# Performance work log

Measured on AMD Instinct MI355X. Metric: run time of the kernel, lower is better.

Reference implementation:

```python
import jax, jax.numpy as jnp
import numpy as np

B, CIN, C, H, W = 2, 64, 128, 64, 1024
H2, W2 = H // 2, W // 2

def _unfold(x, k, pad, stride, dil=1):
    # F.unfold equivalent -> [B, C, k*k, Ho, Wo] with (kh, kw) row-major ordering
    Bx, Cx, Hx, Wx = x.shape
    Ho = (Hx + 2 * pad - dil * (k - 1) - 1) // stride + 1
    Wo = (Wx + 2 * pad - dil * (k - 1) - 1) // stride + 1
    xp = jnp.pad(x, ((0, 0), (0, 0), (pad, pad), (pad, pad)))
    pats = [xp[:, :, i * dil:i * dil + stride * (Ho - 1) + 1:stride,
                  j * dil:j * dil + stride * (Wo - 1) + 1:stride]
            for i in range(k) for j in range(k)]
    return jnp.stack(pats, axis=2)

def _conv(x, w, b, pad, dil=1):
    y = jax.lax.conv_general_dilated(x, w, (1, 1), ((pad, pad), (pad, pad)),
                                     rhs_dilation=(dil, dil),
                                     dimension_numbers=('NCHW', 'OIHW', 'NCHW'))
    return y + b[None, :, None, None]

def _c1x1(x, w, b):
    return jnp.einsum('oi,bi...->bo...', w, x) + b.reshape((1, -1) + (1,) * (x.ndim - 2))

def _bn(x, s, b):
    shp = (1, -1) + (1,) * (x.ndim - 2)
    return x * s.reshape(shp) + b.reshape(shp)

def _forward(x, xyz, c1_w, c1_b, c2_w, c2_b, c3_w, c3_b, c4_w, c4_b, c5_w, c5_b,
             rbn_s, rbn_b, p_w, p_b, pbn_s, pbn_b, lin_w, lin_b,
             w1_w, w1_b, w2_w, w2_b, w3_w, w3_b,
             wbn1_s, wbn1_b, wbn2_s, wbn2_b, wbn3_s, wbn3_b):
    lrelu, relu = jax.nn.leaky_relu, jax.nn.relu
    # get_group_mask geometry (kernel 5, stride 2): relative neighbor coordinates
    gxyz = _unfold(xyz, 5, 2, 2) - xyz[:, :, ::2, ::2][:, :, None]  # [B,3,25,H2,W2]
    # ResBlock trunk (eval-mode BN folded to per-channel scale/shift)
    shortcut = lrelu(_c1x1(x, c1_w, c1_b))
    resA1 = _bn(lrelu(_conv(x, c2_w, c2_b, pad=1)), rbn_s[0], rbn_b[0])
    resA2 = _bn(lrelu(_conv(resA1, c3_w, c3_b, pad=2, dil=2)), rbn_s[1], rbn_b[1])
    resA3 = _bn(lrelu(_conv(resA2, c4_w, c4_b, pad=1, dil=2)), rbn_s[2], rbn_b[2])
    concat = jnp.concatenate([resA1, resA2, resA3], axis=1)
    resA = _bn(lrelu(_c1x1(concat, c5_w, c5_b)), rbn_s[3], rbn_b[3]) + shortcut
    # PConv downsample: pointwise MLP, WeightNet on geometry, unfold + per-pixel matmul
    h = resA
    for i in range(3):
        h = relu(_bn(_c1x1(h, p_w[i], p_b[i]), pbn_s[i], pbn_b[i]))
    wn = relu(_bn(_c1x1(gxyz, w1_w, w1_b), wbn1_s, wbn1_b))
    wn = relu(_bn(_c1x1(wn, w2_w, w2_b), wbn2_s, wbn2_b))
    wn = relu(_bn(_c1x1(wn, w3_w, w3_b), wbn3_s, wbn3_b))          # [B,16,25,H2,W2]
    unf = _unfold(h, 5, 2, 2)                                      # [B,C,25,H2,W2]
    y = jnp.einsum('bckhw,bnkhw->bcnhw', unf, wn).reshape(B, C * 16, H2, W2)
    resB = relu(_bn(_c1x1(y, lin_w, lin_b), pbn_s[3], pbn_b[3]))   # [B,C,H2,W2]
    return resB, resA

def setup_inputs():
    keys = iter(jax.random.split(jax.random.key(0), 48))
    def rn(shape, scale=0.05):
        return jax.random.normal(next(keys), shape, jnp.float32) * scale
    def bn_pair(shape):
        return 1.0 + rn(shape, 0.1), rn(shape, 0.1)
    d = {}
    d['x'] = rn((B, CIN, H, W), 1.0)
    d['xyz'] = rn((B, 3, H, W), 0.1)
    d['c1_w'], d['c1_b'] = rn((C, CIN)), rn((C,))
    d['c2_w'], d['c2_b'] = rn((C, CIN, 3, 3)), rn((C,))
    d['c3_w'], d['c3_b'] = rn((C, C, 3, 3)), rn((C,))
    d['c4_w'], d['c4_b'] = rn((C, C, 2, 2)), rn((C,))
    d['c5_w'], d['c5_b'] = rn((C, 3 * C)), rn((C,))
    d['rbn_s'], d['rbn_b'] = bn_pair((4, C))
    d['p_w'], d['p_b'] = rn((3, C, C)), rn((3, C))
    d['pbn_s'], d['pbn_b'] = bn_pair((4, C))
    d['lin_w'], d['lin_b'] = rn((C, 16 * C), 0.02), rn((C,))
    d['w1_w'], d['w1_b'] = rn((8, 3), 0.5), rn((8,))
    d['w2_w'], d['w2_b'] = rn((8, 8), 0.5), rn((8,))
    d['w3_w'], d['w3_b'] = rn((16, 8), 0.5), rn((16,))
    d['wbn1_s'], d['wbn1_b'] = bn_pair((8,))
    d['wbn2_s'], d['wbn2_b'] = bn_pair((8,))
    d['wbn3_s'], d['wbn3_b'] = bn_pair((16,))
    return d

def reference(x, xyz, c1_w, c1_b, c2_w, c2_b, c3_w, c3_b, c4_w, c4_b, c5_w, c5_b,
              rbn_s, rbn_b, p_w, p_b, pbn_s, pbn_b, lin_w, lin_b,
              w1_w, w1_b, w2_w, w2_b, w3_w, w3_b,
              wbn1_s, wbn1_b, wbn2_s, wbn2_b, wbn3_s, wbn3_b):
    return _forward(x, xyz, c1_w, c1_b, c2_w, c2_b, c3_w, c3_b, c4_w, c4_b, c5_w, c5_b,
                    rbn_s, rbn_b, p_w, p_b, pbn_s, pbn_b, lin_w, lin_b,
                    w1_w, w1_b, w2_w, w2_b, w3_w, w3_b,
                    wbn1_s, wbn1_b, wbn2_s, wbn2_b, wbn3_s, wbn3_b)
```

## Files before the change

### kernel.cpp

```cpp
#include <hip/hip_runtime.h>
#include <hip/hip_bf16.h>

typedef __hip_bfloat16 bf16;
typedef unsigned short u16;
typedef unsigned int   u32;

#define B_   2
#define CIN_ 64
#define C_   128
#define H_   64
#define W_   1024
#define HW_  (H_*W_)
#define H2_  32
#define W2_  512
#define HW2_ (H2_*W2_)

typedef __attribute__((ext_vector_type(8))) short bf16x8;
typedef __attribute__((ext_vector_type(4))) float f32x4;

#define OFF_C2  0
#define OFF_C3  73728
#define OFF_C4  221184
#define OFF_C5  286720
#define OFF_C1  335872
#define OFF_PW  344064
#define OFF_LIN 393216
#define WTS_TOT 655360
__device__ __align__(16) u16 g_wts[WTS_TOT];
__device__ __align__(16) u16 g_b1[(size_t)B_*C_*HW_];
__device__ __align__(16) u16 g_b2[(size_t)B_*C_*HW_];
__device__ __align__(16) u16 g_b3[(size_t)B_*C_*HW_];
__device__ __align__(16) u16 g_xb[(size_t)B_*HW_*CIN_];

__device__ __forceinline__ float bits2f(u16 u){
    u32 x = ((u32)u) << 16; float f; __builtin_memcpy(&f, &x, 4); return f;
}
__device__ __forceinline__ u16 f2bits(float v){
    bf16 h = __float2bfloat16(v); u16 u; __builtin_memcpy(&u, &h, 2); return u;
}
__device__ __forceinline__ float lrelu(float v){ return v > 0.f ? v : 0.01f*v; }
__device__ __forceinline__ float relu (float v){ return v > 0.f ? v : 0.f; }

#define LSTR 40
#define PSTR 136
#define TSTR 136

__device__ __forceinline__ void stage_A(u16* As, const u16* w, int wstr, int col0, int tid)
{
#pragma unroll
    for (int r = 0; r < 2; r++) {
        int e = tid + 256*r;
        int co = e >> 2, ch = e & 3;
        *(uint4*)&As[co*LSTR + ch*8] = *(const uint4*)&w[co*wstr + col0 + ch*8];
    }
}

__device__ __forceinline__ void stage_B_pm(u16* Bs, const u16* src, int rowStride,
                                           int kc, int tid)
{
#pragma unroll
    for (int r = 0; r < 2; r++) {
        int e = tid + 256*r;
        int j = e >> 2, g = e & 3;
        *(uint4*)&Bs[j*LSTR + g*8] =
            *(const uint4*)&src[(size_t)j*rowStride + kc*32 + g*8];
    }
}

__device__ __forceinline__ void mfma_step_s(const u16* As, const u16* Bs, int bstr, int koff,
                                            int lane, int wm, int wn_, f32x4 acc[4][4])
{
    const int quad = lane >> 4, l15 = lane & 15;
    bf16x8 a[4], b[4];
#pragma unroll
    for (int i = 0; i < 4; i++)
        a[i] = *(const bf16x8*)&As[(wm*64 + i*16 + l15)*LSTR + quad*8];
#pragma unroll
    for (int j = 0; j < 4; j++)
        b[j] = *(const bf16x8*)&Bs[(wn_*64 + j*16 + l15)*bstr + koff + quad*8];
#pragma unroll
    for (int i = 0; i < 4; i++)
#pragma unroll
        for (int j = 0; j < 4; j++)
            acc[i][j] = __builtin_amdgcn_mfma_f32_16x16x32_bf16(a[i], b[j], acc[i][j], 0, 0, 0);
}

__device__ __forceinline__ void mfma_step(const u16* As, const u16* Bs,
                                          int lane, int wm, int wn_, f32x4 acc[4][4])
{
    mfma_step_s(As, Bs, LSTR, 0, lane, wm, wn_, acc);
}

__device__ __forceinline__ void init_bias(f32x4 acc[4][4], const float* bias, int wm, int lane)
{
    const int quad = lane >> 4;
#pragma unroll
    for (int i = 0; i < 4; i++)
#pragma unroll
        for (int r = 0; r < 4; r++) {
            float bv = bias[wm*64 + i*16 + quad*4 + r];
#pragma unroll
            for (int j = 0; j < 4; j++) acc[i][j][r] = bv;
        }
}

#define XTS 70
__global__ __launch_bounds__(256)
void k_xtrans(const float* __restrict__ x0, u16* __restrict__ xb0)
{
    __shared__ __align__(16) u16 T[128*XTS];
    const int tid = threadIdx.x;
    const float* x = x0 + (size_t)blockIdx.y*CIN_*HW_;
    u16* xb = xb0 + (size_t)blockIdx.y*HW_*CIN_;
    const int pix0 = blockIdx.x * 128;
#pragma unroll
    for (int r = 0; r < 8; r++) {
        int e = tid + 256*r;
        int c = e >> 5, p4 = (e & 31)*4;
        float4 v = *(const float4*)&x[(size_t)c*HW_ + pix0 + p4];
        T[(p4+0)*XTS + c] = f2bits(v.x);
        T[(p4+1)*XTS + c] = f2bits(v.y);
        T[(p4+2)*XTS + c] = f2bits(v.z);
        T[(p4+3)*XTS + c] = f2bits(v.w);
    }
    __syncthreads();
#pragma unroll
    for (int r = 0; r < 4; r++) {
        int e = tid + 256*r;
        int p = e >> 3, g = e & 7;
        const u16* s = &T[p*XTS + g*8];
        u16* d = &xb[(size_t)(pix0+p)*CIN_ + g*8];
        *(uint2*)&d[0] = *(const uint2*)&s[0];
        *(uint2*)&d[4] = *(const uint2*)&s[4];
    }
}

template<int CI, int KS, int DIL, int PAD>
__global__ __launch_bounds__(256)
void k_conv(const u16* __restrict__ in0, const u16* __restrict__ wT,
            const float* __restrict__ bias, const float* __restrict__ bns,
            const float* __restrict__ bnb, u16* __restrict__ out0)
{
    constexpr int WTOT = 136;
    constexpr int ASZ  = KS*128*LSTR;
    constexpr int SSZ  = (ASZ + WTOT*LSTR) > 128*TSTR ? (ASZ + WTOT*LSTR) : 128*TSTR;
    __shared__ __align__(16) u16 S[SSZ];
    u16* As = S;
    u16* Bs = S + ASZ;
    const int tid = threadIdx.x, lane = tid & 63, wave = tid >> 6;
    const int wm = wave & 1, wn_ = wave >> 1;
    const int quad = lane >> 4, l15 = lane & 15;
    const u16* in = in0 + (size_t)blockIdx.y*HW_*CI;
    u16* out = out0 + (size_t)blockIdx.y*HW_*C_;
    const int pix0 = blockIdx.x * 128;
    const int y = pix0 >> 10, x0 = pix0 & 1023;

    f32x4 acc[4][4];
    init_bias(acc, bias, wm, lane);

    for (int dyi = 0; dyi < KS; dyi++) {
        int yy = y + dyi*DIL - PAD;
        if (yy < 0 || yy >= H_) continue;
        const u16* srow = in + (size_t)yy*W_*CI;
        for (int kc = 0; kc < CI/32; kc++) {
            __syncthreads();
            for (int e = tid; e < KS*512; e += 256) {
                int d = e >> 9, rem = e & 511;
                int co = rem >> 2, ch = rem & 3;
                *(uint4*)&As[d*128*LSTR + co*LSTR + ch*8] =
                    *(const uint4*)&wT[(size_t)(dyi*KS + d)*128*CI + co*CI + kc*32 + ch*8];
            }
            for (int e = tid; e < WTOT*4; e += 256) {
                int wpx = e >> 2, g = e & 3;
                int xx = x0 - PAD + wpx;
                uint4 v = make_uint4(0u, 0u, 0u, 0u);
                if ((unsigned)xx < (unsigned)W_)
                    v = *(const uint4*)&srow[(size_t)xx*CI + kc*32 + g*8];
                *(uint4*)&Bs[wpx*LSTR + g*8] = v;
            }
            __syncthreads();
#pragma unroll
            for (int d = 0; d < KS; d++) {
                bf16x8 a[4], bb[4];
#pragma unroll
                for (int i = 0; i < 4; i++)
                    a[i] = *(const bf16x8*)&As[d*128*LSTR + (wm*64 + i*16 + l15)*LSTR + quad*8];
#pragma unroll
                for (int j = 0; j < 4; j++)
                    bb[j] = *(const bf16x8*)&Bs[(wn_*64 + j*16 + l15 + d*DIL)*LSTR + quad*8];
#pragma unroll
                for (int i = 0; i < 4; i++)
#pragma unroll
                    for (int j = 0; j < 4; j++)
                        acc[i][j] = __builtin_amdgcn_mfma_f32_16x16x32_bf16(a[i], bb[j], acc[i][j], 0, 0, 0);
            }
        }
    }
    u16* T = S;
    __syncthreads();
#pragma unroll
    for (int i = 0; i < 4; i++)
#pragma unroll
        for (int r = 0; r < 4; r++) {
            int co = wm*64 + i*16 + quad*4 + r;
            float ss = bns[co], tt = bnb[co];
#pragma unroll
            for (int j = 0; j < 4; j++) {
                float v = lrelu(acc[i][j][r]) * ss + tt;
                T[(wn_*64 + j*16 + l15)*TSTR + co] = f2bits(v);
            }
        }
    __syncthreads();
#pragma unroll
    for (int r = 0; r < 8; r++) {
        int e = tid + 256*r;
        int px = e >> 4, g = e & 15;
        *(uint4*)&out[(size_t)(pix0+px)*C_ + g*8] = *(const uint4*)&T[px*TSTR + g*8];
    }
}

__global__ __launch_bounds__(256)
void k_resA(const u16* __restrict__ xb0, const u16* __restrict__ a10,
            const u16* __restrict__ a20, const u16* __restrict__ a30,
            const u16* __restrict__ wc1, const float* __restrict__ c1b,
            const u16* __restrict__ wc5, const float* __restrict__ c5b,
            const float* __restrict__ s3, const float* __restrict__ b3,
            float* __restrict__ out0)
{
    __shared__ __align__(16) u16 As[128*LSTR];
    __shared__ __align__(16) u16 Bs[128*LSTR];
    const int tid = threadIdx.x, lane = tid & 63, wave = tid >> 6;
    const int wm = wave & 1, wn_ = wave >> 1;
    const int b = blockIdx.y;
    const u16* xb = xb0 + (size_t)b*HW_*CIN_;
    const u16* aa[3] = { a10 + (size_t)b*HW_*C_, a20 + (size_t)b*HW_*C_, a30 + (size_t)b*HW_*C_ };
    float* out = out0 + (size_t)b*C_*HW_;
    const int pix0 = blockIdx.x * 128;
    const int quad = lane >> 4, l15 = lane & 15;

    f32x4 acc[4][4];
    init_bias(acc, c1b, wm, lane);
    for (int kc = 0; kc < 2; kc++) {
        stage_A(As, wc1, 64, kc*32, tid);
        stage_B_pm(Bs, xb + (size_t)pix0*CIN_, CIN_, kc, tid);
        __syncthreads();
        mfma_step(As, Bs, lane, wm, wn_, acc);
        __syncthreads();
    }
    float sc[4][4][4];
#pragma unroll
    for (int i = 0; i < 4; i++)
#pragma unroll
        for (int j = 0; j < 4; j++)
#pragma unroll
            for (int r = 0; r < 4; r++) sc[i][j][r] = lrelu(acc[i][j][r]);

    init_bias(acc, c5b, wm, lane);
    for (int s = 0; s < 3; s++) {
        const u16* src = aa[s] + (size_t)pix0*C_;
        for (int kc = 0; kc < 4; kc++) {
            stage_A(As, wc5, 384, s*128 + kc*32, tid);
            stage_B_pm(Bs, src, C_, kc, tid);
            __syncthreads();
            mfma_step(As, Bs, lane, wm, wn_, acc);
            __syncthreads();
        }
    }
#pragma unroll
    for (int i = 0; i < 4; i++)
#pragma unroll
        for (int r = 0; r < 4; r++) {
            int co = wm*64 + i*16 + quad*4 + r;
            float ss = s3[co], tt = b3[co];
#pragma unroll
            for (int j = 0; j < 4; j++) {
                float v = lrelu(acc[i][j][r]) * ss + tt + sc[i][j][r];
                out[co*HW_ + pix0 + wn_*64 + j*16 + l15] = v;
            }
        }
}

__global__ __launch_bounds__(256)
void k_pw3(const float* __restrict__ in0, const u16* __restrict__ w,
           const float* __restrict__ pb, const float* __restrict__ ps,
           const float* __restrict__ pbb, u16* __restrict__ out0)
{
    __shared__ __align__(16) u16 As[128*LSTR];
    __shared__ __align__(16) u16 B0[128*PSTR];
    __shared__ __align__(16) u16 B1[128*PSTR];
    const int tid = threadIdx.x, lane = tid & 63, wave = tid >> 6;
    const int wm = wave & 1, wn_ = wave >> 1;
    const int b = blockIdx.y;
    const float* in = in0 + (size_t)b*C_*HW_;
    u16* out = out0 + (size_t)b*C_*HW_;
    const int pix0 = blockIdx.x * 128;
    const int quad = lane >> 4, l15 = lane & 15;

    for (int e = tid; e < 128*32; e += 256) {
        int kk = e >> 5, j4 = (e & 31)*4;
        float4 v = *(const float4*)&in[kk*HW_ + pix0 + j4];
        u16* d = &B0[j4*PSTR + kk];
        d[0]      = f2bits(v.x);
        d[PSTR]   = f2bits(v.y);
        d[2*PSTR] = f2bits(v.z);
        d[3*PSTR] = f2bits(v.w);
    }

    u16* Bc = B0;
    u16* Bn = B1;
#pragma unroll
    for (int L = 0; L < 3; L++) {
        f32x4 acc[4][4];
        init_bias(acc, pb + L*128, wm, lane);
        for (int kc = 0; kc < 4; kc++) {
            stage_A(As, w + L*16384, 128, kc*32, tid);
            __syncthreads();
            mfma_step_s(As, Bc, PSTR, kc*32, lane, wm, wn_, acc);
            __syncthreads();
        }
        const float* ss = ps + L*128;
        const float* tt = pbb + L*128;
        if (L < 2) {
#pragma unroll
            for (int i = 0; i < 4; i++)
#pragma unroll
                for (int r = 0; r < 4; r++) {
                    int co = wm*64 + i*16 + quad*4 + r;
                    float s1 = ss[co], t1 = tt[co];
#pragma unroll
                    for (int j = 0; j < 4; j++) {
                        float v = relu(acc[i][j][r] * s1 + t1);
                        Bn[(wn_*64 + j*16 + l15)*PSTR + co] = f2bits(v);
                    }
                }
            u16* t = Bc; Bc = Bn; Bn = t;
        } else {
#pragma unroll
            for (int i = 0; i < 4; i++)
#pragma unroll
                for (int r = 0; r < 4; r++) {
                    int co = wm*64 + i*16 + quad*4 + r;
                    float s1 = ss[co], t1 = tt[co];
#pragma unroll
                    for (int j = 0; j < 4; j++) {
                        float v = relu(acc[i][j][r] * s1 + t1);
                        out[co*HW_ + pix0 + wn_*64 + j*16 + l15] = f2bits(v);
                    }
                }
        }
    }
}

__global__ __launch_bounds__(256)
void wn_kernel(const float* __restrict__ xyz0,
               const float* __restrict__ w1w, const float* __restrict__ w1b,
               const float* __restrict__ w2w, const float* __restrict__ w2b,
               const float* __restrict__ w3w, const float* __restrict__ w3b,
               const float* __restrict__ s1, const float* __restrict__ bb1,
               const float* __restrict__ s2, const float* __restrict__ bb2,
               const float* __restrict__ s3, const float* __restrict__ bb3,
               u16* __restrict__ out0)
{
    const float* xyz = xyz0 + (size_t)blockIdx.y*3*HW_;
    u16* out = out0 + (size_t)blockIdx.y*400*HW2_;
    int idx = blockIdx.x*256 + threadIdx.x;
    int j = idx & (W2_-1); int t = idx >> 9;
    int i = t & (H2_-1);   int k = t >> 5;
    int kh = k / 5, kw = k - kh*5;
    int yy = 2*i + kh - 2, xx = 2*j + kw - 2;
    bool inr = (yy >= 0 && yy < H_ && xx >= 0 && xx < W_);

    float g[3];
#pragma unroll
    for (int c = 0; c < 3; c++) {
        float ctr = xyz[c*HW_ + (2*i)*W_ + 2*j];
        float v = inr ? xyz[c*HW_ + yy*W_ + xx] : 0.f;
        g[c] = v - ctr;
    }
    float a1[8];
#pragma unroll
    for (int n = 0; n < 8; n++) {
        float v = w1b[n];
#pragma unroll
        for (int c = 0; c < 3; c++) v += w1w[n*3 + c] * g[c];
        a1[n] = relu(v * s1[n] + bb1[n]);
    }
    float a2[8];
#pragma unroll
    for (int n = 0; n < 8; n++) {
        float v = w2b[n];
#pragma unroll
        for (int m = 0; m < 8; m++) v += w2w[n*8 + m] * a1[m];
        a2[n] = relu(v * s2[n] + bb2[n]);
    }
#pragma unroll
    for (int n = 0; n < 16; n++) {
        float v = w3b[n];
#pragma unroll
        for (int m = 0; m < 8; m++) v += w3w[n*8 + m] * a2[m];
        v = relu(v * s3[n] + bb3[n]);
        out[(n*25 + k)*HW2_ + i*W2_ + j] = f2bits(v);
    }
}

__global__ __launch_bounds__(512)
void k_yfused(const u16* __restrict__ h0, const u16* __restrict__ wn0,
              const u16* __restrict__ w, const float* __restrict__ bias,
              const float* __restrict__ bns, const float* __restrict__ bnb,
              float* __restrict__ out0)
{
    __shared__ __align__(16) float slab[40*148];
    __shared__ __align__(16) u16 Bs[64*PSTR];
    const int tid = threadIdx.x;
    const int bx = blockIdx.x;
    const int j0 = (bx & 7) * 64;
    const int i2 = bx >> 3;
    const int b  = blockIdx.y;
    const u16* h  = h0  + (size_t)b*C_*HW_;
    const u16* wn = wn0 + (size_t)b*400*HW2_;
    float* out = out0 + (size_t)b*C_*HW2_;

    const int n = tid & 15, pxq = tid >> 4;
    const int lane = tid & 63, wave = tid >> 6;
    const int wm4 = wave & 3, wnp = wave >> 2;
    const int quad = lane >> 4, l15 = lane & 15;

    float wnreg[25][2];
    {
        const u16* wb = wn + (n*25)*HW2_ + i2*W2_ + j0 + pxq*2;
#pragma unroll
        for (int k = 0; k < 25; k++) {
            u32 t = *(const u32*)(wb + k*HW2_);
            wnreg[k][0] = bits2f((u16)(t & 0xffff));
            wnreg[k][1] = bits2f((u16)(t >> 16));
        }
    }

    const int bA0 = (wm4*32 +  0 + l15)*2048 + quad*8;
    const int bA1 = (wm4*32 + 16 + l15)*2048 + quad*8;

    f32x4 acc[2][2];
#pragma unroll
    for (int i = 0; i < 2; i++)
#pragma unroll
        for (int r = 0; r < 4; r++) {
            float bv = bias[wm4*32 + i*16 + quad*4 + r];
            acc[i][0][r] = bv;
            acc[i][1][r] = bv;
        }

    for (int c0 = 0; c0 < 128; c0 += 8) {
        __syncthreads();
        for (int e = tid; e < 720; e += 512) {
            int cc = e / 90, rem = e - cc*90;
            int rr = rem / 18, g = rem - rr*18;
            int yy = 2*i2 + rr - 2;
            int xs0 = 2*j0 - 8 + 8*g;
            float f[8];
            if ((unsigned)yy < (unsigned)H_ && (unsigned)xs0 <= (unsigned)(W_-8)) {
                uint4 v = *(const uint4*)&h[(c0+cc)*HW_ + yy*W_ + xs0];
                f[0] = bits2f((u16)(v.x & 0xffff)); f[1] = bits2f((u16)(v.x >> 16));
                f[2] = bits2f((u16)(v.y & 0xffff)); f[3] = bits2f((u16)(v.y >> 16));
                f[4] = bits2f((u16)(v.z & 0xffff)); f[5] = bits2f((u16)(v.z >> 16));
                f[6] = bits2f((u16)(v.w & 0xffff)); f[7] = bits2f((u16)(v.w >> 16));
            } else if ((unsigned)yy < (unsigned)H_) {
#pragma unroll
                for (int m = 0; m < 8; m++) {
                    int xs = xs0 + m;
                    f[m] = ((unsigned)xs < (unsigned)W_)
                         ? bits2f(h[(c0+cc)*HW_ + yy*W_ + xs]) : 0.f;
                }
            } else {
#pragma unroll
                for (int m = 0; m < 8; m++) f[m] = 0.f;
            }
            float* d = &slab[(cc*5 + rr)*148 + 2 + 8*g];
            *(float2*)(d+0) = make_float2(f[0], f[1]);
            *(float2*)(d+2) = make_float2(f[2], f[3]);
            *(float2*)(d+4) = make_float2(f[4], f[5]);
            *(float2*)(d+6) = make_float2(f[6], f[7]);
        }
        bf16x8 af0[4], af1[4];
#pragma unroll
        for (int kc = 0; kc < 4; kc++) {
            af0[kc] = *(const bf16x8*)&w[bA0 + c0*16 + kc*32];
            af1[kc] = *(const bf16x8*)&w[bA1 + c0*16 + kc*32];
        }
        __syncthreads();
#pragma unroll 2
        for (int cc = 0; cc < 8; cc++) {
            float yv0 = 0.f, yv1 = 0.f;
#pragma unroll
            for (int rr = 0; rr < 5; rr++) {
                const float* fr = &slab[(cc*5 + rr)*148 + 8 + 4*pxq];
                float4 A  = *(const float4*)fr;
                float4 Bv = *(const float4*)(fr + 4);
                yv0 += A.x*wnreg[rr*5+0][0] + A.y*wnreg[rr*5+1][0]
                     + A.z*wnreg[rr*5+2][0] + A.w*wnreg[rr*5+3][0]
                     + Bv.x*wnreg[rr*5+4][0];
                yv1 += A.z*wnreg[rr*5+0][1] + A.w*wnreg[rr*5+1][1]
                     + Bv.x*wnreg[rr*5+2][1] + Bv.y*wnreg[rr*5+3][1]
                     + Bv.z*wnreg[rr*5+4][1];
            }
            Bs[(2*pxq)  *PSTR + cc*16 + n] = f2bits(yv0);
            Bs[(2*pxq+1)*PSTR + cc*16 + n] = f2bits(yv1);
        }
        __syncthreads();
#pragma unroll
        for (int kc = 0; kc < 4; kc++) {
            bf16x8 b0 = *(const bf16x8*)&Bs[(wnp*32 +  0 + l15)*PSTR + kc*32 + quad*8];
            bf16x8 b1 = *(const bf16x8*)&Bs[(wnp*32 + 16 + l15)*PSTR + kc*32 + quad*8];
            acc[0][0] = __builtin_amdgcn_mfma_f32_16x16x32_bf16(af0[kc], b0, acc[0][0], 0, 0, 0);
            acc[0][1] = __builtin_amdgcn_mfma_f32_16x16x32_bf16(af0[kc], b1, acc[0][1], 0, 0, 0);
            acc[1][0] = __builtin_amdgcn_mfma_f32_16x16x32_bf16(af1[kc], b0, acc[1][0], 0, 0, 0);
            acc[1][1] = __builtin_amdgcn_mfma_f32_16x16x32_bf16(af1[kc], b1, acc[1][1], 0, 0, 0);
        }
    }
#pragma unroll
    for (int i = 0; i < 2; i++)
#pragma unroll
        for (int r = 0; r < 4; r++) {
            int co = wm4*32 + i*16 + quad*4 + r;
            float ss = bns[co], tt = bnb[co];
#pragma unroll
            for (int j = 0; j < 2; j++) {
                float v = relu(acc[i][j][r] * ss + tt);
                out[co*HW2_ + i2*W2_ + j0 + wnp*32 + j*16 + l15] = v;
            }
        }
}

__global__ __launch_bounds__(256)
void k_wtrans(const float* __restrict__ c2w, const float* __restrict__ c3w,
              const float* __restrict__ c4w, const float* __restrict__ c5w,
              const float* __restrict__ c1w, const float* __restrict__ pw,
              const float* __restrict__ linw)
{
    int i = blockIdx.x*256 + threadIdx.x;
    if (i >= WTS_TOT) return;
    float v;
    if (i < OFF_C3) {
        int p = i / 8192, rem = i - p*8192;
        int co = rem >> 6, ci = rem & 63;
        v = c2w[(co*64 + ci)*9 + p];
    } else if (i < OFF_C4) {
        int t = i - OFF_C3;
        int p = t / 16384, rem = t - p*16384;
        int co = rem >> 7, ci = rem & 127;
        v = c3w[(co*128 + ci)*9 + p];
    } else if (i < OFF_C5) {
        int t = i - OFF_C4;
        int p = t / 16384, rem = t - p*16384;
        int co = rem >> 7, ci = rem & 127;
        v = c4w[(co*128 + ci)*4 + p];
    } else if (i < OFF_C1)  v = c5w[i - OFF_C5];
    else if (i < OFF_PW)    v = c1w[i - OFF_C1];
    else if (i < OFF_LIN)   v = pw[i - OFF_PW];
    else                    v = linw[i - OFF_LIN];
    g_wts[i] = f2bits(v);
}

extern "C" void kernel_launch(void* const* d_in, const int* in_sizes, int n_in,
                              void* d_out, int out_size, void* d_ws, size_t ws_size,
                              hipStream_t stream)
{
    const float* x     = (const float*)d_in[0];
    const float* xyz   = (const float*)d_in[1];
    const float* c1_w  = (const float*)d_in[2];
    const float* c1_b  = (const float*)d_in[3];
    const float* c2_w  = (const float*)d_in[4];
    const float* c2_b  = (const float*)d_in[5];
    const float* c3_w  = (const float*)d_in[6];
    const float* c3_b  = (const float*)d_in[7];
    const float* c4_w  = (const float*)d_in[8];
    const float* c4_b  = (const float*)d_in[9];
    const float* c5_w  = (const float*)d_in[10];
    const float* c5_b  = (const float*)d_in[11];
    const float* rbn_s = (const float*)d_in[12];
    const float* rbn_b = (const float*)d_in[13];
    const float* p_w   = (const float*)d_in[14];
    const float* p_b   = (const float*)d_in[15];
    const float* pbn_s = (const float*)d_in[16];
    const float* pbn_b = (const float*)d_in[17];
    const float* lin_w = (const float*)d_in[18];
    const float* lin_b = (const float*)d_in[19];
    const float* w1_w  = (const float*)d_in[20];
    const float* w1_b  = (const float*)d_in[21];
    const float* w2_w  = (const float*)d_in[22];
    const float* w2_b  = (const float*)d_in[23];
    const float* w3_w  = (const float*)d_in[24];
    const float* w3_b  = (const float*)d_in[25];
    const float* wbn1_s = (const float*)d_in[26];
    const float* wbn1_b = (const float*)d_in[27];
    const float* wbn2_s = (const float*)d_in[28];
    const float* wbn2_b = (const float*)d_in[29];
    const float* wbn3_s = (const float*)d_in[30];
    const float* wbn3_b = (const float*)d_in[31];

    float* outB = (float*)d_out;
    float* outA = outB + (size_t)B_*C_*HW2_;

    u16 *wts, *b1, *b2, *b3, *xb;
    { void* p; hipGetSymbolAddress(&p, HIP_SYMBOL(g_wts)); wts = (u16*)p; }
    { void* p; hipGetSymbolAddress(&p, HIP_SYMBOL(g_b1));  b1  = (u16*)p; }
    { void* p; hipGetSymbolAddress(&p, HIP_SYMBOL(g_b2));  b2  = (u16*)p; }
    { void* p; hipGetSymbolAddress(&p, HIP_SYMBOL(g_b3));  b3  = (u16*)p; }
    { void* p; hipGetSymbolAddress(&p, HIP_SYMBOL(g_xb));  xb  = (u16*)p; }

    dim3 blk(256);

    k_wtrans<<<dim3((WTS_TOT + 255)/256), blk, 0, stream>>>(c2_w, c3_w, c4_w, c5_w,
                                                            c1_w, p_w, lin_w);
    k_xtrans<<<dim3(512, B_), blk, 0, stream>>>(x, xb);
    k_conv<64,3,1,1><<<dim3(512, B_), blk, 0, stream>>>(xb, wts+OFF_C2, c2_b,
                                                        rbn_s, rbn_b, b1);
    k_conv<128,3,2,2><<<dim3(512, B_), blk, 0, stream>>>(b1, wts+OFF_C3, c3_b,
                                                         rbn_s+128, rbn_b+128, b2);
    k_conv<128,2,2,1><<<dim3(512, B_), blk, 0, stream>>>(b2, wts+OFF_C4, c4_b,
                                                         rbn_s+256, rbn_b+256, b3);
    k_resA<<<dim3(512, B_), blk, 0, stream>>>(xb, b1, b2, b3, wts+OFF_C1, c1_b,
                                              wts+OFF_C5, c5_b, rbn_s+384, rbn_b+384, outA);
    k_pw3<<<dim3(512, B_), blk, 0, stream>>>(outA, wts+OFF_PW, p_b, pbn_s, pbn_b, b1);
    wn_kernel<<<dim3(1600, B_), blk, 0, stream>>>(xyz, w1_w, w1_b, w2_w, w2_b, w3_w, w3_b,
                                                  wbn1_s, wbn1_b, wbn2_s, wbn2_b,
                                                  wbn3_s, wbn3_b, b2);
    k_yfused<<<dim3(256, B_), dim3(512), 0, stream>>>(b1, b2, wts+OFF_LIN, lin_b,
                                                      pbn_s+384, pbn_b+384, outB);
}
```

Measured before the change: 570.0 us.

## Double-buffer the input slab in k_yfused and prefetch the next channel group

The per-channel-group slab in k_yfused now lives in two shared-memory buffers. The global loads for the next 8 channels are issued into registers before the current group's weighted-sum and MFMA work, and written to the other buffer afterwards, so load latency can overlap compute. Slab address and bounds math is hoisted out of the loop, and the partial-boundary element-wise load path is dropped because chunks are always fully in or fully out of range. The weight fragment loads are split into two halves to spread register pressure. The cost is double the slab LDS footprint, which may reduce how many blocks fit per CU, plus an extra barrier per iteration.

```diff
diff --git a/kernel.cpp b/kernel.cpp
--- a/kernel.cpp
+++ b/kernel.cpp
@@ -403,13 +403,21 @@
     }
 }
 
+__device__ __forceinline__ void yf_wr8(float* d, uint4 v)
+{
+    *(float2*)(d+0) = make_float2(bits2f((u16)(v.x & 0xffff)), bits2f((u16)(v.x >> 16)));
+    *(float2*)(d+2) = make_float2(bits2f((u16)(v.y & 0xffff)), bits2f((u16)(v.y >> 16)));
+    *(float2*)(d+4) = make_float2(bits2f((u16)(v.z & 0xffff)), bits2f((u16)(v.z >> 16)));
+    *(float2*)(d+6) = make_float2(bits2f((u16)(v.w & 0xffff)), bits2f((u16)(v.w >> 16)));
+}
+
 __global__ __launch_bounds__(512)
 void k_yfused(const u16* __restrict__ h0, const u16* __restrict__ wn0,
               const u16* __restrict__ w, const float* __restrict__ bias,
               const float* __restrict__ bns, const float* __restrict__ bnb,
               float* __restrict__ out0)
 {
-    __shared__ __align__(16) float slab[40*148];
+    __shared__ __align__(16) float slab[2][40*148];
     __shared__ __align__(16) u16 Bs[64*PSTR];
     const int tid = threadIdx.x;
     const int bx = blockIdx.x;
@@ -425,6 +433,21 @@
     const int wm4 = wave & 3, wnp = wave >> 2;
     const int quad = lane >> 4, l15 = lane & 15;
 
+    const int e0 = tid;
+    const int cc0 = e0/90, r0 = e0 - cc0*90, rr0 = r0/18, g0 = r0 - rr0*18;
+    const int yy0 = 2*i2 + rr0 - 2, xa0 = 2*j0 - 8 + 8*g0;
+    const bool ok0 = ((unsigned)yy0 < (unsigned)H_) && ((unsigned)xa0 <= (unsigned)(W_-8));
+    const int src0 = cc0*HW_ + yy0*W_ + xa0;
+    const int dst0 = (cc0*5 + rr0)*148 + 2 + 8*g0;
+
+    const int e1 = tid + 512;
+    const bool has1 = (e1 < 720);
+    const int cc1 = e1/90, r1 = e1 - cc1*90, rr1 = r1/18, g1 = r1 - rr1*18;
+    const int yy1 = 2*i2 + rr1 - 2, xa1 = 2*j0 - 8 + 8*g1;
+    const bool ok1 = has1 && ((unsigned)yy1 < (unsigned)H_) && ((unsigned)xa1 <= (unsigned)(W_-8));
+    const int src1 = cc1*HW_ + yy1*W_ + xa1;
+    const int dst1 = (cc1*5 + rr1)*148 + 2 + 8*g1;
+
     float wnreg[25][2];
     {
         const u16* wb = wn + (n*25)*HW2_ + i2*W2_ + j0 + pxq*2;
@@ -449,50 +472,39 @@
             acc[i][1][r] = bv;
         }
 
-    for (int c0 = 0; c0 < 128; c0 += 8) {
-        __syncthreads();
-        for (int e = tid; e < 720; e += 512) {
-            int cc = e / 90, rem = e - cc*90;
-            int rr = rem / 18, g = rem - rr*18;
-            int yy = 2*i2 + rr - 2;
-            int xs0 = 2*j0 - 8 + 8*g;
-            float f[8];
-            if ((unsigned)yy < (unsigned)H_ && (unsigned)xs0 <= (unsigned)(W_-8)) {
-                uint4 v = *(const uint4*)&h[(c0+cc)*HW_ + yy*W_ + xs0];
-                f[0] = bits2f((u16)(v.x & 0xffff)); f[1] = bits2f((u16)(v.x >> 16));
-                f[2] = bits2f((u16)(v.y & 0xffff)); f[3] = bits2f((u16)(v.y >> 16));
-                f[4] = bits2f((u16)(v.z & 0xffff)); f[5] = bits2f((u16)(v.z >> 16));
-                f[6] = bits2f((u16)(v.w & 0xffff)); f[7] = bits2f((u16)(v.w >> 16));
-            } else if ((unsigned)yy < (unsigned)H_) {
-#pragma unroll
-                for (int m = 0; m < 8; m++) {
-                    int xs = xs0 + m;
-                    f[m] = ((unsigned)xs < (unsigned)W_)
-                         ? bits2f(h[(c0+cc)*HW_ + yy*W_ + xs]) : 0.f;
-                }
-            } else {
-#pragma unroll
-                for (int m = 0; m < 8; m++) f[m] = 0.f;
-            }
-            float* d = &slab[(cc*5 + rr)*148 + 2 + 8*g];
-            *(float2*)(d+0) = make_float2(f[0], f[1]);
-            *(float2*)(d+2) = make_float2(f[2], f[3]);
-            *(float2*)(d+4) = make_float2(f[4], f[5]);
-            *(float2*)(d+6) = make_float2(f[6], f[7]);
-        }
-        bf16x8 af0[4], af1[4];
-#pragma unroll
-        for (int kc = 0; kc < 4; kc++) {
-            af0[kc] = *(const bf16x8*)&w[bA0 + c0*16 + kc*32];
-            af1[kc] = *(const bf16x8*)&w[bA1 + c0*16 + kc*32];
-        }
-        __syncthreads();
+    {
+        uint4 v0 = make_uint4(0u,0u,0u,0u), v1 = make_uint4(0u,0u,0u,0u);
+        if (ok0) v0 = *(const uint4*)&h[src0];
+        if (ok1) v1 = *(const uint4*)&h[src1];
+        yf_wr8(&slab[0][dst0], v0);
+        if (has1) yf_wr8(&slab[0][dst1], v1);
+    }
+    __syncthreads();
+
+    for (int t = 0; t < 16; t++) {
+        const int c0 = t*8;
+        const float* scur = slab[t & 1];
+        float* snxt = slab[(t & 1) ^ 1];
+
+        uint4 v0 = make_uint4(0u,0u,0u,0u), v1 = make_uint4(0u,0u,0u,0u);
+        if (t < 15) {
+            const int ch = (c0 + 8)*HW_;
+            if (ok0) v0 = *(const uint4*)&h[src0 + ch];
+            if (ok1) v1 = *(const uint4*)&h[src1 + ch];
+        }
+        bf16x8 afA[2][2];
+#pragma unroll
+        for (int kc = 0; kc < 2; kc++) {
+            afA[0][kc] = *(const bf16x8*)&w[bA0 + c0*16 + kc*32];
+            afA[1][kc] = *(const bf16x8*)&w[bA1 + c0*16 + kc*32];
+        }
+
 #pragma unroll 2
         for (int cc = 0; cc < 8; cc++) {
             float yv0 = 0.f, yv1 = 0.f;
 #pragma unroll
             for (int rr = 0; rr < 5; rr++) {
-                const float* fr = &slab[(cc*5 + rr)*148 + 8 + 4*pxq];
+                const float* fr = &scur[(cc*5 + rr)*148 + 8 + 4*pxq];
                 float4 A  = *(const float4*)fr;
                 float4 Bv = *(const float4*)(fr + 4);
                 yv0 += A.x*wnreg[rr*5+0][0] + A.y*wnreg[rr*5+1][0]
@@ -506,15 +518,29 @@
             Bs[(2*pxq+1)*PSTR + cc*16 + n] = f2bits(yv1);
         }
         __syncthreads();
+
+        bf16x8 afB[2][2];
+#pragma unroll
+        for (int kc = 0; kc < 2; kc++) {
+            afB[0][kc] = *(const bf16x8*)&w[bA0 + c0*16 + (kc+2)*32];
+            afB[1][kc] = *(const bf16x8*)&w[bA1 + c0*16 + (kc+2)*32];
+        }
+        if (t < 15) {
+            yf_wr8(&snxt[dst0], v0);
+            if (has1) yf_wr8(&snxt[dst1], v1);
+        }
 #pragma unroll
         for (int kc = 0; kc < 4; kc++) {
             bf16x8 b0 = *(const bf16x8*)&Bs[(wnp*32 +  0 + l15)*PSTR + kc*32 + quad*8];
             bf16x8 b1 = *(const bf16x8*)&Bs[(wnp*32 + 16 + l15)*PSTR + kc*32 + quad*8];
-            acc[0][0] = __builtin_amdgcn_mfma_f32_16x16x32_bf16(af0[kc], b0, acc[0][0], 0, 0, 0);
-            acc[0][1] = __builtin_amdgcn_mfma_f32_16x16x32_bf16(af0[kc], b1, acc[0][1], 0, 0, 0);
-            acc[1][0] = __builtin_amdgcn_mfma_f32_16x16x32_bf16(af1[kc], b0, acc[1][0], 0, 0, 0);
-            acc[1][1] = __builtin_amdgcn_mfma_f32_16x16x32_bf16(af1[kc], b1, acc[1][1], 0, 0, 0);
-        }
+            bf16x8 a0 = (kc < 2) ? afA[0][kc] : afB[0][kc-2];
+            bf16x8 a1 = (kc < 2) ? afA[1][kc] : afB[1][kc-2];
+            acc[0][0] = __builtin_amdgcn_mfma_f32_16x16x32_bf16(a0, b0, acc[0][0], 0, 0, 0);
+            acc[0][1] = __builtin_amdgcn_mfma_f32_16x16x32_bf16(a0, b1, acc[0][1], 0, 0, 0);
+            acc[1][0] = __builtin_amdgcn_mfma_f32_16x16x32_bf16(a1, b0, acc[1][0], 0, 0, 0);
+            acc[1][1] = __builtin_amdgcn_mfma_f32_16x16x32_bf16(a1, b1, acc[1][1], 0, 0, 0);
+        }
+        __syncthreads();
     }
 #pragma unroll
     for (int i = 0; i < 2; i++)
```

Result: faster. 528.2 us (-7.3%).
